# Optimization experiments

Measured on AMD Instinct MI355X. Metric: run time of the kernel, lower is better.

## Reference

```python
import jax, jax.numpy as jnp
import numpy as np

N, IN_DIM, OUT_DIM, H = 8192, 512, 512, 1
BN_EPS = 1e-5


def _lin(key, fan_in, fan_out):
    k1, k2 = jax.random.split(key)
    b = 1.0 / np.sqrt(fan_in)
    W = jax.random.uniform(k1, (fan_in, fan_out), jnp.float32, -b, b)
    bias = jax.random.uniform(k2, (fan_out,), jnp.float32, -b, b)
    return W, bias


def setup_inputs() -> dict:
    key = jax.random.key(0)
    ks = jax.random.split(key, 12)
    h = jax.random.normal(ks[0], (N, IN_DIM), jnp.float32)
    A = (jax.random.uniform(ks[1], (N, N)) < 0.01).astype(jnp.float32)
    qw, qb = _lin(ks[2], IN_DIM, OUT_DIM * H)
    kw, kb = _lin(ks[3], IN_DIM, OUT_DIM * H)
    vw, vb = _lin(ks[4], IN_DIM, OUT_DIM * H)
    ow, ob = _lin(ks[5], OUT_DIM, OUT_DIM)
    f1w, f1b = _lin(ks[6], OUT_DIM, OUT_DIM * 2)
    f2w, f2b = _lin(ks[7], OUT_DIM * 2, OUT_DIM)
    bn1_g = jax.random.normal(ks[8], (OUT_DIM,)) * 0.1 + 1.0
    bn1_b = jax.random.normal(ks[9], (OUT_DIM,)) * 0.1
    bn1_m = jax.random.normal(ks[10], (OUT_DIM,)) * 0.1
    bn1_v = jax.random.uniform(ks[11], (OUT_DIM,), jnp.float32, 0.5, 1.5)
    ks2 = jax.random.split(jax.random.fold_in(key, 7), 4)
    bn2_g = jax.random.normal(ks2[0], (OUT_DIM,)) * 0.1 + 1.0
    bn2_b = jax.random.normal(ks2[1], (OUT_DIM,)) * 0.1
    bn2_m = jax.random.normal(ks2[2], (OUT_DIM,)) * 0.1
    bn2_v = jax.random.uniform(ks2[3], (OUT_DIM,), jnp.float32, 0.5, 1.5)
    return dict(A=A, h=h, qw=qw, qb=qb, kw=kw, kb=kb, vw=vw, vb=vb,
                ow=ow, ob=ob, f1w=f1w, f1b=f1b, f2w=f2w, f2b=f2b,
                bn1_g=bn1_g, bn1_b=bn1_b, bn1_m=bn1_m, bn1_v=bn1_v,
                bn2_g=bn2_g, bn2_b=bn2_b, bn2_m=bn2_m, bn2_v=bn2_v)


def _bn_eval(x, g, b, m, v):
    return (x - m) * jax.lax.rsqrt(v + BN_EPS) * g + b


def reference(A, h, qw, qb, kw, kb, vw, vb, ow, ob, f1w, f1b, f2w, f2b,
              bn1_g, bn1_b, bn1_m, bn1_v, bn2_g, bn2_b, bn2_m, bn2_v):
    n = h.shape[0]
    scaling = OUT_DIM ** (-0.5)
    # q/k/v: [N, D, H] as in torch reshape of [N, D*H]
    q = (h @ qw + qb).reshape(n, OUT_DIM, H) * scaling
    k = (h @ kw + kb).reshape(n, OUT_DIM, H)
    v = (h @ vw + vb).reshape(n, OUT_DIM, H)
    qh = jnp.transpose(q, (2, 0, 1))          # (H, N, D)
    kh = jnp.transpose(k, (2, 1, 0))          # (H, D, N)
    vh = jnp.transpose(v, (2, 0, 1))          # (H, N, D)
    attn = jnp.einsum('hnd,hdm->hnm', qh, kh) * A[None]   # (H, N, N)
    attn = jax.nn.softmax(attn, axis=0)        # NOTE: softmax over HEAD axis, as in source
    out = jnp.einsum('hnm,hmd->hnd', attn, vh).reshape(n, H * OUT_DIM)
    # GTLayer (eval mode: dropout = identity, BN uses running stats)
    x = out @ ow + ob
    x = x + h                                  # residual
    x = _bn_eval(x, bn1_g, bn1_b, bn1_m, bn1_v)
    h2 = x
    f = jax.nn.relu(x @ f1w + f1b) @ f2w + f2b
    x = h2 + f
    x = _bn_eval(x, bn2_g, bn2_b, bn2_m, bn2_v)
    return x
```

## Files before the change

kernel.cpp:

```cpp
#include <hip/hip_runtime.h>

#define NROWS 8192
#define DIM 512
#define HID 1024
#define BN_EPS 1e-5f

typedef unsigned short ushort_t;
typedef __attribute__((ext_vector_type(8))) __bf16 bf16x8;
typedef __attribute__((ext_vector_type(4))) float f32x4;

union U4 {
    uint4 u;
    bf16x8 b;
    ushort_t s[8];
};

static __device__ __forceinline__ float b2f(ushort_t u) {
    union { float f; unsigned int i; } c;
    c.i = ((unsigned int)u) << 16;
    return c.f;
}

static __device__ __forceinline__ ushort_t f2b(float f) {
    union { float f; unsigned int i; } c;
    c.f = f;
    unsigned int i = c.i;
    unsigned int r = (i + 0x7FFFu + ((i >> 16) & 1u)) >> 16;
    return (ushort_t)r;
}

__global__ void colsum_kernel(const float* __restrict__ h, float* __restrict__ hs) {
    int t = threadIdx.x;
    int col0 = (t & 127) * 4;
    int rsub = t >> 7;
    int row0 = blockIdx.x * 128;
    float acc[4] = {0.f, 0.f, 0.f, 0.f};
    for (int r = 0; r < 64; ++r) {
        int row = row0 + r * 2 + rsub;
        float4 v = *(const float4*)(h + row * DIM + col0);
        acc[0] += v.x; acc[1] += v.y; acc[2] += v.z; acc[3] += v.w;
    }
#pragma unroll
    for (int j = 0; j < 4; ++j) atomicAdd(&hs[col0 + j], acc[j]);
}

__global__ void matvec_kernel(const float* __restrict__ xin, const float* __restrict__ W,
                              const float* __restrict__ bvec, float scaleB,
                              float* __restrict__ outv) {
    __shared__ float red[8][32];
    int t = threadIdx.x;
    int col = blockIdx.x * 32 + (t & 31);
    int ks = t >> 5;
    float s = 0.f;
    for (int ki = 0; ki < 64; ++ki) {
        int k = ks * 64 + ki;
        s += xin[k] * W[k * 512 + col];
    }
    red[ks][t & 31] = s;
    __syncthreads();
    if (ks == 0) {
        float tot = scaleB * bvec[col];
#pragma unroll
        for (int r = 0; r < 8; ++r) tot += red[r][t & 31];
        outv[col] = tot;
    }
}

__global__ void prep_const_kernel(const float* __restrict__ tvec,
                                  const float* g1, const float* b1,
                                  const float* m1, const float* v1,
                                  const float* g2, const float* b2,
                                  const float* m2, const float* v2,
                                  float* __restrict__ p, float* __restrict__ q0,
                                  float* __restrict__ a2v, float* __restrict__ c2v) {
    int d = threadIdx.x;
    float a1 = g1[d] * rsqrtf(v1[d] + BN_EPS);
    float c1 = b1[d] - m1[d] * a1;
    p[d] = a1;
    q0[d] = tvec[d] * a1 + c1;
    float a2 = g2[d] * rsqrtf(v2[d] + BN_EPS);
    a2v[d] = a2;
    c2v[d] = b2[d] - m2[d] * a2;
}

__global__ void x1_kernel(const float* __restrict__ h, const float* __restrict__ p,
                          const float* __restrict__ q0, ushort_t* __restrict__ x1) {
    int idx = (blockIdx.x * blockDim.x + threadIdx.x) * 4;
    int d0 = idx & (DIM - 1);
    float4 hv = *(const float4*)(h + idx);
    ushort_t ov[4];
    ov[0] = f2b(hv.x * p[d0 + 0] + q0[d0 + 0]);
    ov[1] = f2b(hv.y * p[d0 + 1] + q0[d0 + 1]);
    ov[2] = f2b(hv.z * p[d0 + 2] + q0[d0 + 2]);
    ov[3] = f2b(hv.w * p[d0 + 3] + q0[d0 + 3]);
    *(uint2*)(x1 + idx) = *(uint2*)ov;
}

__global__ void transpose_kernel(const float* __restrict__ in, ushort_t* __restrict__ out,
                                 int R, int C) {
    __shared__ float tile[32][33];
    int tx = threadIdx.x & 31, ty = threadIdx.x >> 5;
    int bx = blockIdx.x * 32, by = blockIdx.y * 32;
#pragma unroll
    for (int i = 0; i < 32; i += 8)
        tile[ty + i][tx] = in[(by + ty + i) * C + bx + tx];
    __syncthreads();
#pragma unroll
    for (int i = 0; i < 32; i += 8)
        out[(bx + ty + i) * R + by + tx] = f2b(tile[tx][ty + i]);
}

template <bool RELU>
__global__ __launch_bounds__(256) void gemm_kernel(const ushort_t* __restrict__ A,
                                                   const ushort_t* __restrict__ BT,
                                                   const float* __restrict__ bias,
                                                   ushort_t* __restrict__ C, int M, int Nn, int K) {
    const int BK = 32, LDA = BK + 8;
    __shared__ ushort_t As[128 * LDA];
    __shared__ ushort_t Bs[128 * LDA];
    int tid = threadIdx.x;
    int lane = tid & 63, w = tid >> 6;
    int wm = (w & 1) * 64, wn = (w >> 1) * 64;
    int bm = blockIdx.y * 128, bn = blockIdx.x * 128;

    f32x4 acc[4][4] = {};

    int c0 = tid, c1 = tid + 256;
    int r0 = c0 >> 2, kc0 = (c0 & 3) * 8;
    int r1 = c1 >> 2, kc1 = (c1 & 3) * 8;

    for (int k0 = 0; k0 < K; k0 += BK) {
        __syncthreads();
        uint4 a0 = *(const uint4*)(A + (size_t)(bm + r0) * K + k0 + kc0);
        uint4 a1 = *(const uint4*)(A + (size_t)(bm + r1) * K + k0 + kc1);
        uint4 b0 = *(const uint4*)(BT + (size_t)(bn + r0) * K + k0 + kc0);
        uint4 b1 = *(const uint4*)(BT + (size_t)(bn + r1) * K + k0 + kc1);
        *(uint4*)(As + r0 * LDA + kc0) = a0;
        *(uint4*)(As + r1 * LDA + kc1) = a1;
        *(uint4*)(Bs + r0 * LDA + kc0) = b0;
        *(uint4*)(Bs + r1 * LDA + kc1) = b1;
        __syncthreads();

        int koff = (lane >> 4) * 8;
        bf16x8 af[4], bfr[4];
#pragma unroll
        for (int i = 0; i < 4; ++i) {
            U4 t;
            t.u = *(const uint4*)(As + (wm + i * 16 + (lane & 15)) * LDA + koff);
            af[i] = t.b;
        }
#pragma unroll
        for (int j = 0; j < 4; ++j) {
            U4 t;
            t.u = *(const uint4*)(Bs + (wn + j * 16 + (lane & 15)) * LDA + koff);
            bfr[j] = t.b;
        }
#pragma unroll
        for (int i = 0; i < 4; ++i)
#pragma unroll
            for (int j = 0; j < 4; ++j)
                acc[i][j] = __builtin_amdgcn_mfma_f32_16x16x32_bf16(af[i], bfr[j], acc[i][j], 0, 0, 0);
    }

#pragma unroll
    for (int i = 0; i < 4; ++i) {
        int row0 = bm + wm + i * 16 + (lane >> 4) * 4;
#pragma unroll
        for (int j = 0; j < 4; ++j) {
            int col = bn + wn + j * 16 + (lane & 15);
            float bv = bias[col];
#pragma unroll
            for (int r = 0; r < 4; ++r) {
                float v = acc[i][j][r] + bv;
                if (RELU) v = fmaxf(v, 0.f);
                C[(size_t)(row0 + r) * Nn + col] = f2b(v);
            }
        }
    }
}

__global__ void final_kernel(const float* __restrict__ h, const ushort_t* __restrict__ F,
                             const float* __restrict__ p, const float* __restrict__ q0,
                             const float* __restrict__ a2v, const float* __restrict__ c2v,
                             float* __restrict__ out) {
    int idx = (blockIdx.x * blockDim.x + threadIdx.x) * 4;
    int d0 = idx & (DIM - 1);
    float4 hv = *(const float4*)(h + idx);
    ushort_t fv[4];
    *(uint2*)fv = *(const uint2*)(F + idx);
    float4 ov;
    ov.x = ((hv.x * p[d0 + 0] + q0[d0 + 0]) + b2f(fv[0])) * a2v[d0 + 0] + c2v[d0 + 0];
    ov.y = ((hv.y * p[d0 + 1] + q0[d0 + 1]) + b2f(fv[1])) * a2v[d0 + 1] + c2v[d0 + 1];
    ov.z = ((hv.z * p[d0 + 2] + q0[d0 + 2]) + b2f(fv[2])) * a2v[d0 + 2] + c2v[d0 + 2];
    ov.w = ((hv.w * p[d0 + 3] + q0[d0 + 3]) + b2f(fv[3])) * a2v[d0 + 3] + c2v[d0 + 3];
    *(float4*)(out + idx) = ov;
}

extern "C" void kernel_launch(void* const* d_in, const int* in_sizes, int n_in,
                              void* d_out, int out_size, void* d_ws, size_t ws_size,
                              hipStream_t stream) {
    const float* h = (const float*)d_in[1];
    const float* vw = (const float*)d_in[6];
    const float* vb = (const float*)d_in[7];
    const float* ow = (const float*)d_in[8];
    const float* ob = (const float*)d_in[9];
    const float* f1w = (const float*)d_in[10];
    const float* f1b = (const float*)d_in[11];
    const float* f2w = (const float*)d_in[12];
    const float* f2b = (const float*)d_in[13];
    const float* g1 = (const float*)d_in[14];
    const float* b1 = (const float*)d_in[15];
    const float* m1 = (const float*)d_in[16];
    const float* v1 = (const float*)d_in[17];
    const float* g2 = (const float*)d_in[18];
    const float* b2 = (const float*)d_in[19];
    const float* m2 = (const float*)d_in[20];
    const float* v2 = (const float*)d_in[21];
    float* out = (float*)d_out;

    char* ws = (char*)d_ws;
    float* hs = (float*)(ws + 0);
    float* pC = (float*)(ws + 2048);
    float* q0C = (float*)(ws + 4096);
    float* a2C = (float*)(ws + 6144);
    float* c2C = (float*)(ws + 8192);
    float* sBuf = (float*)(ws + 10240);
    float* tBuf = (float*)(ws + 12288);
    ushort_t* X1 = (ushort_t*)(ws + 16384);
    ushort_t* Z = X1 + (size_t)NROWS * DIM;
    ushort_t* F = Z + (size_t)NROWS * HID;
    ushort_t* W1T = F + (size_t)NROWS * DIM;
    ushort_t* W2T = W1T + (size_t)HID * DIM;

    hipMemsetAsync(hs, 0, 512 * sizeof(float), stream);
    colsum_kernel<<<64, 256, 0, stream>>>(h, hs);
    matvec_kernel<<<16, 256, 0, stream>>>(hs, vw, vb, 8192.0f, sBuf);
    matvec_kernel<<<16, 256, 0, stream>>>(sBuf, ow, ob, 1.0f, tBuf);
    prep_const_kernel<<<1, 512, 0, stream>>>(tBuf, g1, b1, m1, v1, g2, b2, m2, v2,
                                             pC, q0C, a2C, c2C);
    x1_kernel<<<4096, 256, 0, stream>>>(h, pC, q0C, X1);
    transpose_kernel<<<dim3(32, 16), 256, 0, stream>>>(f1w, W1T, 512, 1024);
    transpose_kernel<<<dim3(16, 32), 256, 0, stream>>>(f2w, W2T, 1024, 512);
    gemm_kernel<true><<<dim3(8, 64), 256, 0, stream>>>(X1, W1T, f1b, Z, NROWS, HID, DIM);
    gemm_kernel<false><<<dim3(4, 64), 256, 0, stream>>>(Z, W2T, f2b, F, NROWS, DIM, HID);
    final_kernel<<<4096, 256, 0, stream>>>(h, F, pC, q0C, a2C, c2C, out);
}
```

Measured before the change: 436.2 us.

## Fuse BN epilogue into FFN GEMM, use direct-to-LDS loads, merge prep kernels

The final elementwise kernel is folded into the second GEMM's epilogue, so the bf16 F buffer no longer makes a round trip through memory. The second matvec is merged with the BN-constant prep kernel, which saves a launch. Both GEMMs now stage tiles with global_load_lds and BK=64, and the second GEMM uses 64-wide N tiles to launch more blocks. Colsum and x1 also get smaller tweaks: more blocks with an in-block reduction before the atomic, and 8-wide vectorized stores. The unpadded LDS layout may cause bank conflicts on fragment reads, and the fused epilogue writes fp32 with strided h reads.

```diff
diff --git a/kernel.cpp b/kernel.cpp
--- a/kernel.cpp
+++ b/kernel.cpp
@@ -29,19 +29,33 @@
     return (ushort_t)r;
 }
 
+static __device__ __forceinline__ void gload_lds16(const ushort_t* g, ushort_t* l) {
+    __builtin_amdgcn_global_load_lds((const __attribute__((address_space(1))) void*)g,
+                                     (__attribute__((address_space(3))) void*)l, 16, 0, 0);
+}
+
 __global__ void colsum_kernel(const float* __restrict__ h, float* __restrict__ hs) {
+    __shared__ float red[512];
     int t = threadIdx.x;
     int col0 = (t & 127) * 4;
     int rsub = t >> 7;
-    int row0 = blockIdx.x * 128;
+    int row0 = blockIdx.x * 32;
     float acc[4] = {0.f, 0.f, 0.f, 0.f};
-    for (int r = 0; r < 64; ++r) {
+#pragma unroll
+    for (int r = 0; r < 16; ++r) {
         int row = row0 + r * 2 + rsub;
-        float4 v = *(const float4*)(h + row * DIM + col0);
+        float4 v = *(const float4*)(h + (size_t)row * DIM + col0);
         acc[0] += v.x; acc[1] += v.y; acc[2] += v.z; acc[3] += v.w;
     }
-#pragma unroll
-    for (int j = 0; j < 4; ++j) atomicAdd(&hs[col0 + j], acc[j]);
+    if (rsub) {
+#pragma unroll
+        for (int j = 0; j < 4; ++j) red[col0 + j] = acc[j];
+    }
+    __syncthreads();
+    if (!rsub) {
+#pragma unroll
+        for (int j = 0; j < 4; ++j) atomicAdd(&hs[col0 + j], acc[j] + red[col0 + j]);
+    }
 }
 
 __global__ void matvec_kernel(const float* __restrict__ xin, const float* __restrict__ W,
@@ -66,34 +80,55 @@
     }
 }
 
-__global__ void prep_const_kernel(const float* __restrict__ tvec,
-                                  const float* g1, const float* b1,
-                                  const float* m1, const float* v1,
-                                  const float* g2, const float* b2,
-                                  const float* m2, const float* v2,
-                                  float* __restrict__ p, float* __restrict__ q0,
-                                  float* __restrict__ a2v, float* __restrict__ c2v) {
-    int d = threadIdx.x;
-    float a1 = g1[d] * rsqrtf(v1[d] + BN_EPS);
-    float c1 = b1[d] - m1[d] * a1;
-    p[d] = a1;
-    q0[d] = tvec[d] * a1 + c1;
-    float a2 = g2[d] * rsqrtf(v2[d] + BN_EPS);
-    a2v[d] = a2;
-    c2v[d] = b2[d] - m2[d] * a2;
+__global__ void matvec_prep_kernel(const float* __restrict__ xin, const float* __restrict__ W,
+                                   const float* __restrict__ bvec,
+                                   const float* g1, const float* b1,
+                                   const float* m1, const float* v1,
+                                   const float* g2, const float* b2,
+                                   const float* m2, const float* v2,
+                                   float* __restrict__ p, float* __restrict__ q0,
+                                   float* __restrict__ a2v, float* __restrict__ c2v) {
+    __shared__ float red[8][32];
+    int t = threadIdx.x;
+    int col = blockIdx.x * 32 + (t & 31);
+    int ks = t >> 5;
+    float s = 0.f;
+    for (int ki = 0; ki < 64; ++ki) {
+        int k = ks * 64 + ki;
+        s += xin[k] * W[k * 512 + col];
+    }
+    red[ks][t & 31] = s;
+    __syncthreads();
+    if (ks == 0) {
+        float tot = bvec[col];
+#pragma unroll
+        for (int r = 0; r < 8; ++r) tot += red[r][t & 31];
+        float a1 = g1[col] * rsqrtf(v1[col] + BN_EPS);
+        float c1 = b1[col] - m1[col] * a1;
+        p[col] = a1;
+        q0[col] = tot * a1 + c1;
+        float a2 = g2[col] * rsqrtf(v2[col] + BN_EPS);
+        a2v[col] = a2;
+        c2v[col] = b2[col] - m2[col] * a2;
+    }
 }
 
 __global__ void x1_kernel(const float* __restrict__ h, const float* __restrict__ p,
                           const float* __restrict__ q0, ushort_t* __restrict__ x1) {
-    int idx = (blockIdx.x * blockDim.x + threadIdx.x) * 4;
+    int idx = (blockIdx.x * blockDim.x + threadIdx.x) * 8;
     int d0 = idx & (DIM - 1);
-    float4 hv = *(const float4*)(h + idx);
-    ushort_t ov[4];
-    ov[0] = f2b(hv.x * p[d0 + 0] + q0[d0 + 0]);
-    ov[1] = f2b(hv.y * p[d0 + 1] + q0[d0 + 1]);
-    ov[2] = f2b(hv.z * p[d0 + 2] + q0[d0 + 2]);
-    ov[3] = f2b(hv.w * p[d0 + 3] + q0[d0 + 3]);
-    *(uint2*)(x1 + idx) = *(uint2*)ov;
+    float4 h0 = *(const float4*)(h + idx);
+    float4 h1 = *(const float4*)(h + idx + 4);
+    U4 o;
+    o.s[0] = f2b(h0.x * p[d0 + 0] + q0[d0 + 0]);
+    o.s[1] = f2b(h0.y * p[d0 + 1] + q0[d0 + 1]);
+    o.s[2] = f2b(h0.z * p[d0 + 2] + q0[d0 + 2]);
+    o.s[3] = f2b(h0.w * p[d0 + 3] + q0[d0 + 3]);
+    o.s[4] = f2b(h1.x * p[d0 + 4] + q0[d0 + 4]);
+    o.s[5] = f2b(h1.y * p[d0 + 5] + q0[d0 + 5]);
+    o.s[6] = f2b(h1.z * p[d0 + 6] + q0[d0 + 6]);
+    o.s[7] = f2b(h1.w * p[d0 + 7] + q0[d0 + 7]);
+    *(uint4*)(x1 + idx) = o.u;
 }
 
 __global__ void transpose_kernel(const float* __restrict__ in, ushort_t* __restrict__ out,
@@ -110,90 +145,97 @@
         out[(bx + ty + i) * R + by + tx] = f2b(tile[tx][ty + i]);
 }
 
-template <bool RELU>
-__global__ __launch_bounds__(256) void gemm_kernel(const ushort_t* __restrict__ A,
-                                                   const ushort_t* __restrict__ BT,
-                                                   const float* __restrict__ bias,
-                                                   ushort_t* __restrict__ C, int M, int Nn, int K) {
-    const int BK = 32, LDA = BK + 8;
-    __shared__ ushort_t As[128 * LDA];
-    __shared__ ushort_t Bs[128 * LDA];
+template <int ROWS>
+static __device__ __forceinline__ void stage_tile(const ushort_t* __restrict__ g, int ldg,
+                                                  ushort_t* lds, int tid) {
+#pragma unroll
+    for (int it = 0; it < (ROWS * 8) / 256; ++it) {
+        int c = it * 256 + tid;
+        int row = c >> 3;
+        int kc = (c & 7) << 3;
+        const ushort_t* gp = g + (size_t)row * ldg + kc;
+        ushort_t* lp = lds + ((it * 256 + (tid & 192)) << 3);
+        gload_lds16(gp, lp);
+    }
+}
+
+template <int NJ, bool RELU, bool FUSE>
+__global__ __launch_bounds__(256) void gemm_kernel(
+    const ushort_t* __restrict__ A, const ushort_t* __restrict__ BT,
+    const float* __restrict__ bias, ushort_t* __restrict__ Cb,
+    float* __restrict__ Cf, int M, int Nn, int K,
+    const float* __restrict__ h, const float* __restrict__ p,
+    const float* __restrict__ q0, const float* __restrict__ a2,
+    const float* __restrict__ c2) {
+    constexpr int BN = NJ * 32;
+    constexpr int BK = 64;
+    __shared__ ushort_t As[128 * BK];
+    __shared__ ushort_t Bs[BN * BK];
     int tid = threadIdx.x;
     int lane = tid & 63, w = tid >> 6;
-    int wm = (w & 1) * 64, wn = (w >> 1) * 64;
-    int bm = blockIdx.y * 128, bn = blockIdx.x * 128;
-
-    f32x4 acc[4][4] = {};
-
-    int c0 = tid, c1 = tid + 256;
-    int r0 = c0 >> 2, kc0 = (c0 & 3) * 8;
-    int r1 = c1 >> 2, kc1 = (c1 & 3) * 8;
+    int wm = (w & 1) * 64, wn = (w >> 1) * (NJ * 16);
+    int bm = blockIdx.y * 128, bn = blockIdx.x * BN;
+
+    f32x4 acc[4][NJ] = {};
+
+    const ushort_t* Ag = A + (size_t)bm * K;
+    const ushort_t* Bg = BT + (size_t)bn * K;
 
     for (int k0 = 0; k0 < K; k0 += BK) {
         __syncthreads();
-        uint4 a0 = *(const uint4*)(A + (size_t)(bm + r0) * K + k0 + kc0);
-        uint4 a1 = *(const uint4*)(A + (size_t)(bm + r1) * K + k0 + kc1);
-        uint4 b0 = *(const uint4*)(BT + (size_t)(bn + r0) * K + k0 + kc0);
-        uint4 b1 = *(const uint4*)(BT + (size_t)(bn + r1) * K + k0 + kc1);
-        *(uint4*)(As + r0 * LDA + kc0) = a0;
-        *(uint4*)(As + r1 * LDA + kc1) = a1;
-        *(uint4*)(Bs + r0 * LDA + kc0) = b0;
-        *(uint4*)(Bs + r1 * LDA + kc1) = b1;
+        stage_tile<128>(Ag + k0, K, As, tid);
+        stage_tile<BN>(Bg + k0, K, Bs, tid);
         __syncthreads();
-
-        int koff = (lane >> 4) * 8;
-        bf16x8 af[4], bfr[4];
-#pragma unroll
-        for (int i = 0; i < 4; ++i) {
-            U4 t;
-            t.u = *(const uint4*)(As + (wm + i * 16 + (lane & 15)) * LDA + koff);
-            af[i] = t.b;
+#pragma unroll
+        for (int ks = 0; ks < 2; ++ks) {
+            int koff = ks * 32 + (lane >> 4) * 8;
+            bf16x8 af[4], bfr[NJ];
+#pragma unroll
+            for (int i = 0; i < 4; ++i) {
+                U4 t;
+                t.u = *(const uint4*)(As + (wm + i * 16 + (lane & 15)) * BK + koff);
+                af[i] = t.b;
+            }
+#pragma unroll
+            for (int j = 0; j < NJ; ++j) {
+                U4 t;
+                t.u = *(const uint4*)(Bs + (wn + j * 16 + (lane & 15)) * BK + koff);
+                bfr[j] = t.b;
+            }
+#pragma unroll
+            for (int i = 0; i < 4; ++i)
+#pragma unroll
+                for (int j = 0; j < NJ; ++j)
+                    acc[i][j] = __builtin_amdgcn_mfma_f32_16x16x32_bf16(af[i], bfr[j], acc[i][j], 0, 0, 0);
         }
-#pragma unroll
-        for (int j = 0; j < 4; ++j) {
-            U4 t;
-            t.u = *(const uint4*)(Bs + (wn + j * 16 + (lane & 15)) * LDA + koff);
-            bfr[j] = t.b;
-        }
-#pragma unroll
-        for (int i = 0; i < 4; ++i)
-#pragma unroll
-            for (int j = 0; j < 4; ++j)
-                acc[i][j] = __builtin_amdgcn_mfma_f32_16x16x32_bf16(af[i], bfr[j], acc[i][j], 0, 0, 0);
     }
 
 #pragma unroll
     for (int i = 0; i < 4; ++i) {
         int row0 = bm + wm + i * 16 + (lane >> 4) * 4;
 #pragma unroll
-        for (int j = 0; j < 4; ++j) {
+        for (int j = 0; j < NJ; ++j) {
             int col = bn + wn + j * 16 + (lane & 15);
             float bv = bias[col];
-#pragma unroll
-            for (int r = 0; r < 4; ++r) {
-                float v = acc[i][j][r] + bv;
-                if (RELU) v = fmaxf(v, 0.f);
-                C[(size_t)(row0 + r) * Nn + col] = f2b(v);
+            if constexpr (FUSE) {
+                float pv = p[col], qv = q0[col], av = a2[col], cv = c2[col];
+#pragma unroll
+                for (int r = 0; r < 4; ++r) {
+                    int row = row0 + r;
+                    float hv = h[(size_t)row * DIM + col];
+                    float x1v = hv * pv + qv;
+                    Cf[(size_t)row * Nn + col] = (x1v + acc[i][j][r] + bv) * av + cv;
+                }
+            } else {
+#pragma unroll
+                for (int r = 0; r < 4; ++r) {
+                    float v = acc[i][j][r] + bv;
+                    if (RELU) v = fmaxf(v, 0.f);
+                    Cb[(size_t)(row0 + r) * Nn + col] = f2b(v);
+                }
             }
         }
     }
-}
-
-__global__ void final_kernel(const float* __restrict__ h, const ushort_t* __restrict__ F,
-                             const float* __restrict__ p, const float* __restrict__ q0,
-                             const float* __restrict__ a2v, const float* __restrict__ c2v,
-                             float* __restrict__ out) {
-    int idx = (blockIdx.x * blockDim.x + threadIdx.x) * 4;
-    int d0 = idx & (DIM - 1);
-    float4 hv = *(const float4*)(h + idx);
-    ushort_t fv[4];
-    *(uint2*)fv = *(const uint2*)(F + idx);
-    float4 ov;
-    ov.x = ((hv.x * p[d0 + 0] + q0[d0 + 0]) + b2f(fv[0])) * a2v[d0 + 0] + c2v[d0 + 0];
-    ov.y = ((hv.y * p[d0 + 1] + q0[d0 + 1]) + b2f(fv[1])) * a2v[d0 + 1] + c2v[d0 + 1];
-    ov.z = ((hv.z * p[d0 + 2] + q0[d0 + 2]) + b2f(fv[2])) * a2v[d0 + 2] + c2v[d0 + 2];
-    ov.w = ((hv.w * p[d0 + 3] + q0[d0 + 3]) + b2f(fv[3])) * a2v[d0 + 3] + c2v[d0 + 3];
-    *(float4*)(out + idx) = ov;
 }
 
 extern "C" void kernel_launch(void* const* d_in, const int* in_sizes, int n_in,
@@ -225,23 +267,23 @@
     float* a2C = (float*)(ws + 6144);
     float* c2C = (float*)(ws + 8192);
     float* sBuf = (float*)(ws + 10240);
-    float* tBuf = (float*)(ws + 12288);
     ushort_t* X1 = (ushort_t*)(ws + 16384);
     ushort_t* Z = X1 + (size_t)NROWS * DIM;
-    ushort_t* F = Z + (size_t)NROWS * HID;
-    ushort_t* W1T = F + (size_t)NROWS * DIM;
+    ushort_t* W1T = Z + (size_t)NROWS * HID;
     ushort_t* W2T = W1T + (size_t)HID * DIM;
 
     hipMemsetAsync(hs, 0, 512 * sizeof(float), stream);
-    colsum_kernel<<<64, 256, 0, stream>>>(h, hs);
+    colsum_kernel<<<256, 256, 0, stream>>>(h, hs);
     matvec_kernel<<<16, 256, 0, stream>>>(hs, vw, vb, 8192.0f, sBuf);
-    matvec_kernel<<<16, 256, 0, stream>>>(sBuf, ow, ob, 1.0f, tBuf);
-    prep_const_kernel<<<1, 512, 0, stream>>>(tBuf, g1, b1, m1, v1, g2, b2, m2, v2,
-                                             pC, q0C, a2C, c2C);
-    x1_kernel<<<4096, 256, 0, stream>>>(h, pC, q0C, X1);
+    matvec_prep_kernel<<<16, 256, 0, stream>>>(sBuf, ow, ob, g1, b1, m1, v1,
+                                               g2, b2, m2, v2, pC, q0C, a2C, c2C);
+    x1_kernel<<<2048, 256, 0, stream>>>(h, pC, q0C, X1);
     transpose_kernel<<<dim3(32, 16), 256, 0, stream>>>(f1w, W1T, 512, 1024);
     transpose_kernel<<<dim3(16, 32), 256, 0, stream>>>(f2w, W2T, 1024, 512);
-    gemm_kernel<true><<<dim3(8, 64), 256, 0, stream>>>(X1, W1T, f1b, Z, NROWS, HID, DIM);
-    gemm_kernel<false><<<dim3(4, 64), 256, 0, stream>>>(Z, W2T, f2b, F, NROWS, DIM, HID);
-    final_kernel<<<4096, 256, 0, stream>>>(h, F, pC, q0C, a2C, c2C, out);
-}
+    gemm_kernel<4, true, false><<<dim3(8, 64), 256, 0, stream>>>(
+        X1, W1T, f1b, Z, nullptr, NROWS, HID, DIM,
+        nullptr, nullptr, nullptr, nullptr, nullptr);
+    gemm_kernel<2, false, true><<<dim3(8, 64), 256, 0, stream>>>(
+        Z, W2T, f2b, nullptr, out, NROWS, DIM, HID,
+        h, pC, q0C, a2C, c2C);
+}
```

Result: no change. 434.3 us (-0.4%).
